# Kernel optimization log

Measured on AMD Instinct MI355X. Metric: run time of the kernel, lower is better.

## Reference

```python
import jax, jax.numpy as jnp
import numpy as np

B, S, H, NH, FF, L, BLK, R = 2, 4096, 768, 12, 3072, 4, 64, 3
NB = S // BLK          # 64 blocks
D = H // NH            # 64 per-head dim
A = 3 + 2 + R          # window(3) + global(2) + random(R) attended blocks
EPS = 1e-12
SCALE = 1.0 / np.sqrt(D).astype(np.float32)


def setup_inputs() -> dict:
    key = jax.random.key(0)
    ks = jax.random.split(key, 12)
    p = lambda k, shp: jax.random.normal(k, shp, jnp.float32) * 0.02
    return {
        "input_ids": jax.random.normal(ks[0], (B, S, 4), jnp.float32),
        "rand_blocks": jax.random.randint(ks[1], (NB, R), 0, NB, jnp.int32),
        "emb_w": p(ks[2], (4, H)), "emb_b": jnp.zeros((H,), jnp.float32),
        "ln1_g": jnp.ones((L, H), jnp.float32), "ln1_b": jnp.zeros((L, H), jnp.float32),
        "wq": p(ks[3], (L, H, H)), "bq": jnp.zeros((L, H), jnp.float32),
        "wk": p(ks[4], (L, H, H)), "bk": jnp.zeros((L, H), jnp.float32),
        "wv": p(ks[5], (L, H, H)), "bv": jnp.zeros((L, H), jnp.float32),
        "wo": p(ks[6], (L, H, H)), "bo": jnp.zeros((L, H), jnp.float32),
        "ln2_g": jnp.ones((L, H), jnp.float32), "ln2_b": jnp.zeros((L, H), jnp.float32),
        "w1": p(ks[7], (L, H, FF)), "b1": jnp.zeros((L, FF), jnp.float32),
        "w2": p(ks[8], (L, FF, H)), "b2": jnp.zeros((L, H), jnp.float32),
        "clf_w": p(ks[9], (H, 4)), "clf_b": jnp.zeros((4,), jnp.float32),
    }


def _ln(x, g, b):
    m = x.mean(-1, keepdims=True)
    v = jnp.var(x, axis=-1, keepdims=True)  # biased var, like torch LayerNorm
    return (x - m) * jax.lax.rsqrt(v + EPS) * g + b


def _attend_idx(rand_blocks):
    # per query block: [i-1, i, i+1] window (edge-clamped), global {0, NB-1}, R random
    ar = jnp.arange(NB)
    win = jnp.stack([jnp.clip(ar - 1, 0, NB - 1), ar, jnp.clip(ar + 1, 0, NB - 1)], 1)
    glb = jnp.broadcast_to(jnp.array([0, NB - 1], jnp.int32), (NB, 2))
    return jnp.concatenate([win.astype(jnp.int32), glb, rand_blocks], 1)  # [NB, A]


def _attn(x, wq, bq, wk, bk, wv, bv, wo, bo, idx):
    def heads(t):  # [B,S,H] -> [B,NH,NB,BLK,D]
        return t.reshape(B, NB, BLK, NH, D).transpose(0, 3, 1, 2, 4)
    q = heads(x @ wq + bq)
    k = heads(x @ wk + bk)
    v = heads(x @ wv + bv)
    kg = k[:, :, idx].reshape(B, NH, NB, A * BLK, D)  # gather attended key blocks
    vg = v[:, :, idx].reshape(B, NH, NB, A * BLK, D)
    s = jnp.einsum('bhnqd,bhnkd->bhnqk', q, kg) * SCALE  # [B,NH,NB,BLK,A*BLK]
    p = jax.nn.softmax(s, axis=-1)
    o = jnp.einsum('bhnqk,bhnkd->bhnqd', p, vg)
    o = o.transpose(0, 2, 3, 1, 4).reshape(B, S, H)
    return o @ wo + bo


def reference(input_ids, rand_blocks, emb_w, emb_b, ln1_g, ln1_b, wq, bq, wk, bk,
              wv, bv, wo, bo, ln2_g, ln2_b, w1, b1, w2, b2, clf_w, clf_b):
    idx = _attend_idx(rand_blocks)
    x = input_ids @ emb_w + emb_b
    for l in range(L):
        h = _ln(x, ln1_g[l], ln1_b[l])
        x = x + _attn(h, wq[l], bq[l], wk[l], bk[l], wv[l], bv[l], wo[l], bo[l], idx)
        h = _ln(x, ln2_g[l], ln2_b[l])
        x = x + (jax.nn.gelu(h @ w1[l] + b1[l], approximate=False) @ w2[l] + b2[l])
    logits = x @ clf_w + clf_b
    return jax.nn.softmax(logits, axis=-1)
```

## Files before the change

### kernel.cpp

```cpp
#include <hip/hip_runtime.h>
#include <math.h>

constexpr int B  = 2;
constexpr int S  = 4096;
constexpr int H  = 768;
constexpr int NH = 12;
constexpr int FF = 3072;
constexpr int L  = 4;
constexpr int R  = 3;
constexpr int NB = 64;
constexpr int AB = 8;
constexpr float SCALE = 0.125f;
constexpr int QKV_N = 3 * H;

constexpr int ROWS = B * S;
constexpr size_t XSZ = (size_t)B * S * H;

typedef short bf16x8 __attribute__((ext_vector_type(8)));
typedef unsigned short u16x8 __attribute__((ext_vector_type(8)));
typedef unsigned short u16x4 __attribute__((ext_vector_type(4)));
typedef float f32x4 __attribute__((ext_vector_type(4)));
typedef unsigned short ushort_t;

__device__ __forceinline__ ushort_t f2b(float f) {
  union { float f; unsigned u; } c; c.f = f;
  unsigned r = c.u + 0x7fffu + ((c.u >> 16) & 1u);
  return (ushort_t)(r >> 16);
}
__device__ __forceinline__ float b2f(ushort_t u) {
  union { float f; unsigned u; } c; c.u = ((unsigned)u) << 16;
  return c.f;
}

__device__ __forceinline__ float gelu_f(float x) {
  float y = 0.7978845608f * x * (1.0f + 0.044715f * x * x);
  float e = __expf(2.0f * y);
  float th = 1.0f - 2.0f / (e + 1.0f);
  return 0.5f * x * (1.0f + th);
}

__device__ __forceinline__ void gload16(const void* g, void* l) {
  __builtin_amdgcn_global_load_lds(
      (const __attribute__((address_space(1))) unsigned int*)g,
      (__attribute__((address_space(3))) unsigned int*)l, 16, 0, 0);
}

template <int N>
__device__ __forceinline__ void waitvm() {
  if constexpr (N == 0)      { asm volatile("s_waitcnt vmcnt(0)" ::: "memory"); }
  else if constexpr (N == 4) { asm volatile("s_waitcnt vmcnt(4)" ::: "memory"); }
  else if constexpr (N == 6) { asm volatile("s_waitcnt vmcnt(6)" ::: "memory"); }
  else                       { asm volatile("s_waitcnt vmcnt(8)" ::: "memory"); }
}

template <int CTRL>
__device__ __forceinline__ float dppmv(float x) {
  union { float f; int i; } c; c.f = x;
  c.i = __builtin_amdgcn_update_dpp(c.i, c.i, CTRL, 0xF, 0xF, true);
  return c.f;
}
__device__ __forceinline__ float redmax16(float x) {
  x = fmaxf(x, dppmv<0xB1>(x));
  x = fmaxf(x, dppmv<0x4E>(x));
  x = fmaxf(x, dppmv<0x124>(x));
  x = fmaxf(x, dppmv<0x128>(x));
  return x;
}
__device__ __forceinline__ float redsum16(float x) {
  x += dppmv<0xB1>(x);
  x += dppmv<0x4E>(x);
  x += dppmv<0x124>(x);
  x += dppmv<0x128>(x);
  return x;
}

__global__ __launch_bounds__(256) void embed_kernel(
    const float* __restrict__ ids, const float* __restrict__ w,
    const float* __restrict__ bvec, ushort_t* __restrict__ x) {
  int idx = blockIdx.x * 256 + threadIdx.x;
  if (idx >= (int)(XSZ / 4)) return;
  int bs = idx / (H / 4);
  int hc = (idx % (H / 4)) * 4;
  f32x4 s = *(const f32x4*)&bvec[hc];
  #pragma unroll
  for (int k = 0; k < 4; ++k) {
    float id = ids[bs * 4 + k];
    f32x4 wv = *(const f32x4*)&w[k * H + hc];
    #pragma unroll
    for (int j = 0; j < 4; ++j) s[j] += id * wv[j];
  }
  u16x4 pk;
  #pragma unroll
  for (int j = 0; j < 4; ++j) pk[j] = f2b(s[j]);
  *(u16x4*)&x[(size_t)bs * H + hc] = pk;
}

__global__ __launch_bounds__(256) void ln_kernel(
    const ushort_t* __restrict__ x, const float* __restrict__ g,
    const float* __restrict__ bvec, ushort_t* __restrict__ out) {
  const int wave = threadIdx.x >> 6, lane = threadIdx.x & 63;
  const int row = blockIdx.x * 4 + wave;
  const ushort_t* xr = x + (size_t)row * H;
  float v[12];
  #pragma unroll
  for (int j = 0; j < 3; ++j) {
    u16x4 a = *(const u16x4*)&xr[lane * 4 + j * 256];
    #pragma unroll
    for (int q = 0; q < 4; ++q) v[j * 4 + q] = b2f(a[q]);
  }
  float s = 0.f, ss = 0.f;
  #pragma unroll
  for (int i = 0; i < 12; ++i) { s += v[i]; ss += v[i] * v[i]; }
  for (int off = 1; off < 64; off <<= 1) {
    s  += __shfl_xor(s,  off);
    ss += __shfl_xor(ss, off);
  }
  float mean = s * (1.0f / H);
  float var  = ss * (1.0f / H) - mean * mean;
  float rstd = rsqrtf(var + 1e-12f);
  ushort_t* orow = out + (size_t)row * H;
  #pragma unroll
  for (int j = 0; j < 3; ++j) {
    f32x4 gv = *(const f32x4*)&g[lane * 4 + j * 256];
    f32x4 bv = *(const f32x4*)&bvec[lane * 4 + j * 256];
    u16x4 pk;
    #pragma unroll
    for (int q = 0; q < 4; ++q)
      pk[q] = f2b((v[j * 4 + q] - mean) * rstd * gv[q] + bv[q]);
    *(u16x4*)&orow[lane * 4 + j * 256] = pk;
  }
}

__global__ __launch_bounds__(256) void tcvt_kernel(
    const float* __restrict__ in, ushort_t* __restrict__ out,
    int K, int N, size_t inZ, size_t outZ) {
  __shared__ float tile[32][33];
  const float* inz = in + blockIdx.z * inZ;
  ushort_t* outz = out + blockIdx.z * outZ;
  int k0 = blockIdx.y * 32, n0 = blockIdx.x * 32;
  int tx = threadIdx.x & 31, ty = threadIdx.x >> 5;
  #pragma unroll
  for (int i = 0; i < 4; ++i) {
    int kk = ty + i * 8;
    tile[kk][tx] = inz[(size_t)(k0 + kk) * N + n0 + tx];
  }
  __syncthreads();
  #pragma unroll
  for (int i = 0; i < 4; ++i) {
    int nn = ty + i * 8;
    outz[(size_t)(n0 + nn) * K + k0 + tx] = f2b(tile[tx][nn]);
  }
}

__global__ __launch_bounds__(256) void concat_bias_kernel(
    const float* __restrict__ bq, const float* __restrict__ bk,
    const float* __restrict__ bv, float* __restrict__ out) {
  int i = blockIdx.x * 256 + threadIdx.x;
  if (i >= L * QKV_N) return;
  int l = i / QKV_N, c = i % QKV_N;
  float val = (c < H) ? bq[l * H + c] : (c < 2 * H) ? bk[l * H + c - H] : bv[l * H + c - 2 * H];
  out[i] = val;
}

template <int BN, int EPI>
__global__ __launch_bounds__(256, (BN == 256 ? 2 : 3)) void bgemm(
    const ushort_t* __restrict__ A, const ushort_t* __restrict__ Wt,
    const float* __restrict__ bias, const ushort_t* __restrict__ res,
    ushort_t* __restrict__ Cb, ushort_t* __restrict__ Cv,
    int M, int N, int K, int ncol) {
  constexpr int LDSB = (128 + BN) * 32;
  constexpr int NLD  = (128 + BN) / 64;
  constexpr int NI   = BN / 32;
  __shared__ ushort_t lds[3 * LDSB];

  const int nwg = (int)gridDim.x;
  const int qq = nwg >> 3, r0 = nwg & 7;
  const int xcd = (int)blockIdx.x & 7, loc = (int)blockIdx.x >> 3;
  const int swz = (xcd < r0 ? xcd * (qq + 1) : r0 * (qq + 1) + (xcd - r0) * qq) + loc;
  const int bm = (swz / ncol) * 128, bn = (swz % ncol) * BN;

  const int t = threadIdx.x;
  const int wid = t >> 6, lane = t & 63;
  const int fcol = lane & 15, fgrp = lane >> 4;
  const int wm = wid >> 1, wn = wid & 1;

  const ushort_t* src[NLD];
  int dst[NLD];
  #pragma unroll
  for (int j = 0; j < NLD; ++j) {
    int idx = j * 2048 + t * 8;
    dst[j] = idx;
    int ch = (idx >> 3) & 3;
    int row;
    const ushort_t* base;
    if (idx < 4096) { row = idx >> 5;           base = A  + (size_t)(bm + row) * K; }
    else            { row = (idx - 4096) >> 5;  base = Wt + (size_t)(bn + row) * K; }
    src[j] = base + ((ch ^ ((row >> 1) & 3)) << 3);
  }

  int aoff[4], boff[NI];
  #pragma unroll
  for (int mi = 0; mi < 4; ++mi) {
    int row = wm * 64 + mi * 16 + fcol;
    aoff[mi] = row * 32 + ((fgrp ^ ((row >> 1) & 3)) << 3);
  }
  #pragma unroll
  for (int ni = 0; ni < NI; ++ni) {
    int row = wn * (BN / 2) + ni * 16 + fcol;
    boff[ni] = 4096 + row * 32 + ((fgrp ^ ((row >> 1) & 3)) << 3);
  }

  f32x4 acc[4][NI] = {};

  #pragma unroll
  for (int j = 0; j < NLD; ++j) gload16(src[j], &lds[dst[j]]);
  #pragma unroll
  for (int j = 0; j < NLD; ++j) gload16(src[j] + 32, &lds[LDSB + dst[j]]);
  int kgl = 64;

#define GEMM_STEP(P, DOSTAGE, WN)                                          \
  {                                                                        \
    waitvm<WN>();                                                          \
    __builtin_amdgcn_sched_barrier(0);                                     \
    __builtin_amdgcn_s_barrier();                                          \
    __builtin_amdgcn_sched_barrier(0);                                     \
    if (DOSTAGE) {                                                         \
      _Pragma("unroll")                                                    \
      for (int j = 0; j < NLD; ++j)                                        \
        gload16(src[j] + kgl, &lds[(((P) + 2) % 3) * LDSB + dst[j]]);      \
      kgl += 32;                                                           \
    }                                                                      \
    bf16x8 af[4], bfr[NI];                                                 \
    _Pragma("unroll")                                                      \
    for (int mi = 0; mi < 4; ++mi)                                         \
      af[mi] = *(const bf16x8*)&lds[(P) * LDSB + aoff[mi]];                \
    _Pragma("unroll")                                                      \
    for (int ni = 0; ni < NI; ++ni)                                        \
      bfr[ni] = *(const bf16x8*)&lds[(P) * LDSB + boff[ni]];               \
    __builtin_amdgcn_s_setprio(1);                                         \
    _Pragma("unroll")                                                      \
    for (int mi = 0; mi < 4; ++mi)                                         \
      _Pragma("unroll")                                                    \
      for (int ni = 0; ni < NI; ++ni)                                      \
        acc[mi][ni] = __builtin_amdgcn_mfma_f32_16x16x32_bf16(             \
            af[mi], bfr[ni], acc[mi][ni], 0, 0, 0);                        \
    __builtin_amdgcn_s_setprio(0);                                         \
  }

  const int NT = K >> 5;
  for (int tau = 0; tau < NT - 3; tau += 3) {
    GEMM_STEP(0, true, NLD)
    GEMM_STEP(1, true, NLD)
    GEMM_STEP(2, true, NLD)
  }
  GEMM_STEP(0, true,  NLD)
  GEMM_STEP(1, false, NLD)
  GEMM_STEP(2, false, 0)
#undef GEMM_STEP

  if (EPI == 0 && bn >= 2 * H) {
    #pragma unroll
    for (int mi = 0; mi < 4; ++mi) {
      const int m = bm + wm * 64 + mi * 16 + fgrp * 4;
      #pragma unroll
      for (int ni = 0; ni < NI; ++ni) {
        const int n = bn + wn * (BN / 2) + ni * 16 + fcol;
        const float bb = bias[n];
        u16x4 pk;
        #pragma unroll
        for (int r = 0; r < 4; ++r) pk[r] = f2b(acc[mi][ni][r] + bb);
        *(u16x4*)&Cv[(size_t)(n - 2 * H) * M + m] = pk;
      }
    }
    return;
  }
  #pragma unroll
  for (int mi = 0; mi < 4; ++mi) {
    const int m = bm + wm * 64 + mi * 16 + fgrp * 4;
    #pragma unroll
    for (int ni = 0; ni < NI; ++ni) {
      const int n = bn + wn * (BN / 2) + ni * 16 + fcol;
      const float bb = bias[n];
      #pragma unroll
      for (int r = 0; r < 4; ++r) {
        float val = acc[mi][ni][r] + bb;
        if (EPI == 1) {
          val += b2f(res[(size_t)(m + r) * N + n]);
          Cb[(size_t)(m + r) * N + n] = f2b(val);
        } else if (EPI == 2) {
          Cb[(size_t)(m + r) * N + n] = f2b(gelu_f(val));
        } else {
          Cb[(size_t)(m + r) * N + n] = f2b(val);
        }
      }
    }
  }
}

__global__ __launch_bounds__(256) void attn_mfma(
    const ushort_t* __restrict__ qkv, const ushort_t* __restrict__ vT,
    const int* __restrict__ rb, ushort_t* __restrict__ ao) {
  __shared__ ushort_t Ks[2][64 * 72];
  __shared__ ushort_t Vt[2][64 * 72];
  __shared__ ushort_t Ps[4][16 * 72];
  const int xb = blockIdx.x;
  const int n = ((xb & 7) << 3) | (xb >> 3);
  const int hh = blockIdx.y, b = blockIdx.z;
  const int t = threadIdx.x;
  const int wid = t >> 6, lane = t & 63;
  const int fcol = lane & 15, fgrp = lane >> 4;
  const int qr0 = n * 64 + wid * 16;

  bf16x8 qf[2];
  #pragma unroll
  for (int kc = 0; kc < 2; ++kc)
    qf[kc] = *(const bf16x8*)&qkv[((size_t)(b * S) + qr0 + fcol) * QKV_N + hh * 64 + kc * 32 + fgrp * 8];

  f32x4 oacc[4] = {};
  float mrow[4], lrow[4];
  #pragma unroll
  for (int r = 0; r < 4; ++r) { mrow[r] = -1e30f; lrow[r] = 0.f; }

  int kbs[AB];
  kbs[0] = (n > 0) ? n - 1 : 0;
  kbs[1] = n;
  kbs[2] = (n < NB - 1) ? n + 1 : NB - 1;
  kbs[3] = 0;
  kbs[4] = NB - 1;
  kbs[5] = rb[n * R + 0];
  kbs[6] = rb[n * R + 1];
  kbs[7] = rb[n * R + 2];

  const ushort_t* kbase = qkv + (size_t)(b * S) * QKV_N + H + hh * 64;
  const ushort_t* vbase = vT + (size_t)(hh * 64) * ROWS + b * S;

  const int srow = t >> 3;
  const int soff = (t & 7) * 8;

  {
    const int kb = kbs[0];
    u16x8 k0 = *(const u16x8*)&kbase[(size_t)(kb * 64 + srow) * QKV_N + soff];
    u16x8 k1 = *(const u16x8*)&kbase[(size_t)(kb * 64 + srow + 32) * QKV_N + soff];
    u16x8 v0 = *(const u16x8*)&vbase[(size_t)srow * ROWS + kb * 64 + soff];
    u16x8 v1 = *(const u16x8*)&vbase[(size_t)(srow + 32) * ROWS + kb * 64 + soff];
    *(u16x8*)&Ks[0][srow * 72 + soff]        = k0;
    *(u16x8*)&Ks[0][(srow + 32) * 72 + soff] = k1;
    *(u16x8*)&Vt[0][srow * 72 + soff]        = v0;
    *(u16x8*)&Vt[0][(srow + 32) * 72 + soff] = v1;
  }
  __syncthreads();

  for (int a = 0; a < AB; ++a) {
    const int buf = a & 1;

    u16x8 pk0, pk1, pv0, pv1;
    if (a + 1 < AB) {
      const int kb = kbs[a + 1];
      pk0 = *(const u16x8*)&kbase[(size_t)(kb * 64 + srow) * QKV_N + soff];
      pk1 = *(const u16x8*)&kbase[(size_t)(kb * 64 + srow + 32) * QKV_N + soff];
      pv0 = *(const u16x8*)&vbase[(size_t)srow * ROWS + kb * 64 + soff];
      pv1 = *(const u16x8*)&vbase[(size_t)(srow + 32) * ROWS + kb * 64 + soff];
    }

    f32x4 sacc[4] = {};
    __builtin_amdgcn_s_setprio(1);
    #pragma unroll
    for (int ni = 0; ni < 4; ++ni)
      #pragma unroll
      for (int kc = 0; kc < 2; ++kc) {
        bf16x8 kf = *(const bf16x8*)&Ks[buf][(ni * 16 + fcol) * 72 + kc * 32 + fgrp * 8];
        sacc[ni] = __builtin_amdgcn_mfma_f32_16x16x32_bf16(qf[kc], kf, sacc[ni], 0, 0, 0);
      }
    __builtin_amdgcn_s_setprio(0);

    #pragma unroll
    for (int ni = 0; ni < 4; ++ni)
      #pragma unroll
      for (int r = 0; r < 4; ++r) sacc[ni][r] *= SCALE;
    #pragma unroll
    for (int r = 0; r < 4; ++r) {
      float tm = fmaxf(fmaxf(sacc[0][r], sacc[1][r]), fmaxf(sacc[2][r], sacc[3][r]));
      tm = redmax16(tm);
      float mn = fmaxf(mrow[r], tm);
      float corr = __expf(mrow[r] - mn);
      mrow[r] = mn;
      float rs = 0.f;
      #pragma unroll
      for (int ni = 0; ni < 4; ++ni) {
        float p = __expf(sacc[ni][r] - mn);
        sacc[ni][r] = p;
        rs += p;
      }
      rs = redsum16(rs);
      lrow[r] = lrow[r] * corr + rs;
      #pragma unroll
      for (int ni = 0; ni < 4; ++ni) oacc[ni][r] *= corr;
    }

    if (a + 1 < AB) {
      *(u16x8*)&Ks[buf ^ 1][srow * 72 + soff]        = pk0;
      *(u16x8*)&Ks[buf ^ 1][(srow + 32) * 72 + soff] = pk1;
      *(u16x8*)&Vt[buf ^ 1][srow * 72 + soff]        = pv0;
      *(u16x8*)&Vt[buf ^ 1][(srow + 32) * 72 + soff] = pv1;
    }

    #pragma unroll
    for (int ni = 0; ni < 4; ++ni)
      #pragma unroll
      for (int r = 0; r < 4; ++r)
        Ps[wid][(fgrp * 4 + r) * 72 + ni * 16 + fcol] = f2b(sacc[ni][r]);

    bf16x8 pa[2];
    #pragma unroll
    for (int kc = 0; kc < 2; ++kc)
      pa[kc] = *(const bf16x8*)&Ps[wid][fcol * 72 + kc * 32 + fgrp * 8];

    __builtin_amdgcn_s_setprio(1);
    #pragma unroll
    for (int kc = 0; kc < 2; ++kc)
      #pragma unroll
      for (int ni = 0; ni < 4; ++ni) {
        bf16x8 vb = *(const bf16x8*)&Vt[buf][(ni * 16 + fcol) * 72 + kc * 32 + fgrp * 8];
        oacc[ni] = __builtin_amdgcn_mfma_f32_16x16x32_bf16(pa[kc], vb, oacc[ni], 0, 0, 0);
      }
    __builtin_amdgcn_s_setprio(0);

    __syncthreads();
  }

  #pragma unroll
  for (int r = 0; r < 4; ++r) {
    float inv = 1.0f / lrow[r];
    int row = qr0 + fgrp * 4 + r;
    #pragma unroll
    for (int ni = 0; ni < 4; ++ni)
      ao[((size_t)(b * S) + row) * H + hh * 64 + ni * 16 + fcol] = f2b(oacc[ni][r] * inv);
  }
}

__global__ __launch_bounds__(64) void clf_kernel(
    const ushort_t* __restrict__ x, const float* __restrict__ w,
    const float* __restrict__ bvec, float* __restrict__ out) {
  int row = blockIdx.x;
  int lane = threadIdx.x;
  const ushort_t* xr = x + (size_t)row * H;
  float p0 = 0.f, p1 = 0.f, p2 = 0.f, p3 = 0.f;
  for (int d = lane; d < H; d += 64) {
    float xv = b2f(xr[d]);
    p0 += xv * w[d * 4 + 0];
    p1 += xv * w[d * 4 + 1];
    p2 += xv * w[d * 4 + 2];
    p3 += xv * w[d * 4 + 3];
  }
  for (int off = 1; off < 64; off <<= 1) {
    p0 += __shfl_xor(p0, off);
    p1 += __shfl_xor(p1, off);
    p2 += __shfl_xor(p2, off);
    p3 += __shfl_xor(p3, off);
  }
  if (lane == 0) {
    float l0 = p0 + bvec[0], l1 = p1 + bvec[1], l2 = p2 + bvec[2], l3 = p3 + bvec[3];
    float mx = fmaxf(fmaxf(l0, l1), fmaxf(l2, l3));
    float e0 = __expf(l0 - mx), e1 = __expf(l1 - mx), e2 = __expf(l2 - mx), e3 = __expf(l3 - mx);
    float inv = 1.0f / (e0 + e1 + e2 + e3);
    out[row * 4 + 0] = e0 * inv;
    out[row * 4 + 1] = e1 * inv;
    out[row * 4 + 2] = e2 * inv;
    out[row * 4 + 3] = e3 * inv;
  }
}

extern "C" void kernel_launch(void* const* d_in, const int* in_sizes, int n_in,
                              void* d_out, int out_size, void* d_ws, size_t ws_size,
                              hipStream_t stream) {
  const float* input_ids = (const float*)d_in[0];
  const int*   rand_bl   = (const int*)  d_in[1];
  const float* emb_w = (const float*)d_in[2];
  const float* emb_b = (const float*)d_in[3];
  const float* ln1_g = (const float*)d_in[4];
  const float* ln1_b = (const float*)d_in[5];
  const float* wq = (const float*)d_in[6];
  const float* bq = (const float*)d_in[7];
  const float* wk = (const float*)d_in[8];
  const float* bk = (const float*)d_in[9];
  const float* wv = (const float*)d_in[10];
  const float* bv = (const float*)d_in[11];
  const float* wo = (const float*)d_in[12];
  const float* bo = (const float*)d_in[13];
  const float* ln2_g = (const float*)d_in[14];
  const float* ln2_b = (const float*)d_in[15];
  const float* w1 = (const float*)d_in[16];
  const float* b1 = (const float*)d_in[17];
  const float* w2 = (const float*)d_in[18];
  const float* b2 = (const float*)d_in[19];
  const float* clf_w = (const float*)d_in[20];
  const float* clf_b = (const float*)d_in[21];

  char* p = (char*)d_ws;
  ushort_t* x    = (ushort_t*)p; p += XSZ * 2;
  ushort_t* h    = (ushort_t*)p; p += XSZ * 2;
  ushort_t* qkv  = (ushort_t*)p; p += (size_t)ROWS * QKV_N * 2;
  ushort_t* ao   = (ushort_t*)p; p += XSZ * 2;
  ushort_t* ff   = qkv;
  ushort_t* vT   = (ushort_t*)p; p += (size_t)H * ROWS * 2;
  ushort_t* qkvT = (ushort_t*)p; p += (size_t)L * QKV_N * H * 2;
  ushort_t* woT  = (ushort_t*)p; p += (size_t)L * H * H * 2;
  ushort_t* w1T  = (ushort_t*)p; p += (size_t)L * H * FF * 2;
  ushort_t* w2T  = (ushort_t*)p; p += (size_t)L * FF * H * 2;
  float*    bqkv = (float*)p;    p += (size_t)L * QKV_N * 4;

  tcvt_kernel<<<dim3(H / 32, H / 32, L), 256, 0, stream>>>(
      wq, qkvT + 0 * H * H, H, H, (size_t)H * H, (size_t)QKV_N * H);
  tcvt_kernel<<<dim3(H / 32, H / 32, L), 256, 0, stream>>>(
      wk, qkvT + 1 * H * H, H, H, (size_t)H * H, (size_t)QKV_N * H);
  tcvt_kernel<<<dim3(H / 32, H / 32, L), 256, 0, stream>>>(
      wv, qkvT + 2 * H * H, H, H, (size_t)H * H, (size_t)QKV_N * H);
  tcvt_kernel<<<dim3(H / 32, H / 32, L), 256, 0, stream>>>(
      wo, woT, H, H, (size_t)H * H, (size_t)H * H);
  tcvt_kernel<<<dim3(FF / 32, H / 32, L), 256, 0, stream>>>(
      w1, w1T, H, FF, (size_t)H * FF, (size_t)H * FF);
  tcvt_kernel<<<dim3(H / 32, FF / 32, L), 256, 0, stream>>>(
      w2, w2T, FF, H, (size_t)FF * H, (size_t)FF * H);
  concat_bias_kernel<<<(L * QKV_N + 255) / 256, 256, 0, stream>>>(bq, bk, bv, bqkv);

  embed_kernel<<<(int)((XSZ / 4 + 255) / 256), 256, 0, stream>>>(input_ids, emb_w, emb_b, x);

  for (int l = 0; l < L; ++l) {
    ln_kernel<<<ROWS / 4, 256, 0, stream>>>(x, ln1_g + l * H, ln1_b + l * H, h);

    bgemm<256, 0><<<(ROWS / 128) * (QKV_N / 256), 256, 0, stream>>>(
        h, qkvT + (size_t)l * QKV_N * H, bqkv + l * QKV_N, nullptr,
        qkv, vT, ROWS, QKV_N, H, QKV_N / 256);

    attn_mfma<<<dim3(NB, NH, B), 256, 0, stream>>>(qkv, vT, rand_bl, ao);

    bgemm<128, 1><<<(ROWS / 128) * (H / 128), 256, 0, stream>>>(
        ao, woT + (size_t)l * H * H, bo + l * H, x, x, nullptr, ROWS, H, H, H / 128);

    ln_kernel<<<ROWS / 4, 256, 0, stream>>>(x, ln2_g + l * H, ln2_b + l * H, h);

    bgemm<256, 2><<<(ROWS / 128) * (FF / 256), 256, 0, stream>>>(
        h, w1T + (size_t)l * H * FF, b1 + l * FF, nullptr,
        ff, nullptr, ROWS, FF, H, FF / 256);

    bgemm<128, 1><<<(ROWS / 128) * (H / 128), 256, 0, stream>>>(
        ff, w2T + (size_t)l * FF * H, b2 + l * H, x, x, nullptr, ROWS, H, FF, H / 128);
  }

  clf_kernel<<<ROWS, 64, 0, stream>>>(x, clf_w, clf_b, (float*)d_out);
}
```

Baseline: 930.9 us.

## Switch GEMM to double-buffered LDS with higher occupancy; vectorize classifier loads

```diff
diff --git a/kernel.cpp b/kernel.cpp
--- a/kernel.cpp
+++ b/kernel.cpp
@@ -45,14 +45,6 @@
       (__attribute__((address_space(3))) unsigned int*)l, 16, 0, 0);
 }
 
-template <int N>
-__device__ __forceinline__ void waitvm() {
-  if constexpr (N == 0)      { asm volatile("s_waitcnt vmcnt(0)" ::: "memory"); }
-  else if constexpr (N == 4) { asm volatile("s_waitcnt vmcnt(4)" ::: "memory"); }
-  else if constexpr (N == 6) { asm volatile("s_waitcnt vmcnt(6)" ::: "memory"); }
-  else                       { asm volatile("s_waitcnt vmcnt(8)" ::: "memory"); }
-}
-
 template <int CTRL>
 __device__ __forceinline__ float dppmv(float x) {
   union { float f; int i; } c; c.f = x;
@@ -163,7 +155,7 @@
 }
 
 template <int BN, int EPI>
-__global__ __launch_bounds__(256, (BN == 256 ? 2 : 3)) void bgemm(
+__global__ __launch_bounds__(256, (BN == 256 ? 3 : 4)) void bgemm(
     const ushort_t* __restrict__ A, const ushort_t* __restrict__ Wt,
     const float* __restrict__ bias, const ushort_t* __restrict__ res,
     ushort_t* __restrict__ Cb, ushort_t* __restrict__ Cv,
@@ -171,7 +163,7 @@
   constexpr int LDSB = (128 + BN) * 32;
   constexpr int NLD  = (128 + BN) / 64;
   constexpr int NI   = BN / 32;
-  __shared__ ushort_t lds[3 * LDSB];
+  __shared__ ushort_t lds[2 * LDSB];
 
   const int nwg = (int)gridDim.x;
   const int qq = nwg >> 3, r0 = nwg & 7;
@@ -214,20 +206,18 @@
 
   #pragma unroll
   for (int j = 0; j < NLD; ++j) gload16(src[j], &lds[dst[j]]);
-  #pragma unroll
-  for (int j = 0; j < NLD; ++j) gload16(src[j] + 32, &lds[LDSB + dst[j]]);
-  int kgl = 64;
-
-#define GEMM_STEP(P, DOSTAGE, WN)                                          \
+  int kgl = 32;
+
+#define GEMM_STEP(P, DOSTAGE)                                              \
   {                                                                        \
-    waitvm<WN>();                                                          \
+    asm volatile("s_waitcnt vmcnt(0)" ::: "memory");                       \
     __builtin_amdgcn_sched_barrier(0);                                     \
     __builtin_amdgcn_s_barrier();                                          \
     __builtin_amdgcn_sched_barrier(0);                                     \
     if (DOSTAGE) {                                                         \
       _Pragma("unroll")                                                    \
       for (int j = 0; j < NLD; ++j)                                        \
-        gload16(src[j] + kgl, &lds[(((P) + 2) % 3) * LDSB + dst[j]]);      \
+        gload16(src[j] + kgl, &lds[((P) ^ 1) * LDSB + dst[j]]);            \
       kgl += 32;                                                           \
     }                                                                      \
     bf16x8 af[4], bfr[NI];                                                 \
@@ -248,14 +238,12 @@
   }
 
   const int NT = K >> 5;
-  for (int tau = 0; tau < NT - 3; tau += 3) {
-    GEMM_STEP(0, true, NLD)
-    GEMM_STEP(1, true, NLD)
-    GEMM_STEP(2, true, NLD)
-  }
-  GEMM_STEP(0, true,  NLD)
-  GEMM_STEP(1, false, NLD)
-  GEMM_STEP(2, false, 0)
+  for (int tau = 0; tau < NT - 2; tau += 2) {
+    GEMM_STEP(0, true)
+    GEMM_STEP(1, true)
+  }
+  GEMM_STEP(0, true)
+  GEMM_STEP(1, false)
 #undef GEMM_STEP
 
   if (EPI == 0 && bn >= 2 * H) {
@@ -444,22 +432,23 @@
   int row = blockIdx.x;
   int lane = threadIdx.x;
   const ushort_t* xr = x + (size_t)row * H;
-  float p0 = 0.f, p1 = 0.f, p2 = 0.f, p3 = 0.f;
-  for (int d = lane; d < H; d += 64) {
-    float xv = b2f(xr[d]);
-    p0 += xv * w[d * 4 + 0];
-    p1 += xv * w[d * 4 + 1];
-    p2 += xv * w[d * 4 + 2];
-    p3 += xv * w[d * 4 + 3];
-  }
-  for (int off = 1; off < 64; off <<= 1) {
-    p0 += __shfl_xor(p0, off);
-    p1 += __shfl_xor(p1, off);
-    p2 += __shfl_xor(p2, off);
-    p3 += __shfl_xor(p3, off);
-  }
+  f32x4 p = {0.f, 0.f, 0.f, 0.f};
+  #pragma unroll
+  for (int j = 0; j < 3; ++j) {
+    u16x4 xv4 = *(const u16x4*)&xr[lane * 4 + j * 256];
+    #pragma unroll
+    for (int q = 0; q < 4; ++q) {
+      float xv = b2f(xv4[q]);
+      f32x4 wv = *(const f32x4*)&w[(lane * 4 + j * 256 + q) * 4];
+      #pragma unroll
+      for (int c = 0; c < 4; ++c) p[c] += xv * wv[c];
+    }
+  }
+  #pragma unroll
+  for (int c = 0; c < 4; ++c)
+    for (int off = 1; off < 64; off <<= 1) p[c] += __shfl_xor(p[c], off);
   if (lane == 0) {
-    float l0 = p0 + bvec[0], l1 = p1 + bvec[1], l2 = p2 + bvec[2], l3 = p3 + bvec[3];
+    float l0 = p[0] + bvec[0], l1 = p[1] + bvec[1], l2 = p[2] + bvec[2], l3 = p[3] + bvec[3];
     float mx = fmaxf(fmaxf(l0, l1), fmaxf(l2, l3));
     float e0 = __expf(l0 - mx), e1 = __expf(l1 - mx), e2 = __expf(l2 - mx), e3 = __expf(l3 - mx);
     float inv = 1.0f / (e0 + e1 + e2 + e3);
```

Result: slower. 2.243 ms (+141.0%).
